# Kernel optimization log

Hardware: AMD Instinct MI355X
Metric: run time of the kernel (lower is better)

The kernel has to match this reference:

```python
import jax, jax.numpy as jnp
import numpy as np

B, T, D = 4, 4096, 4096
G, C, K, M = 1, 4, 128, 32          # num_groups, n_splits, dw_hidden_dim, heads_per_group
I2 = 4                               # qkw inner dim = 2 * dynamic_hidden_dim (dyn_hidden = 32//16 = 2)
EPS = 1.1920929e-07                  # torch F.rms_norm default eps for fp32


def _rms_norm(x):
    # F.rms_norm over last dim, no learned scale
    return x * jax.lax.rsqrt(jnp.mean(x * x, axis=-1, keepdims=True) + EPS)


def setup_inputs() -> dict:
    key = jax.random.key(0)
    k0, k1, k2, k3 = jax.random.split(key, 4)
    dw1_std = np.sqrt(2.0 / (D + K))
    qkw_std = 0.02 / (np.sqrt(2 * 32 * 2) * (32 + 2))
    dd_std = 0.05 * np.sqrt(2.0 / (32 + D))
    return {
        "query_vec": jax.random.normal(k0, (B, T, D), dtype=jnp.float32),
        "dw1": jax.random.normal(k1, (D, G, C, K), dtype=jnp.float32) * dw1_std,
        "qkw": jax.random.normal(k2, (G, C, K, I2, M), dtype=jnp.float32) * qkw_std,
        "dd": jax.random.normal(k3, (D, G, M * C), dtype=jnp.float32) * dd_std,
        "norm_scale": jnp.ones((G,), dtype=jnp.float32) * 0.001,
    }


def reference(query_vec, dw1, qkw, dd, norm_scale):
    # dw_hidden: [B,T,G,C,K]
    dw_hidden = jnp.einsum('btd,dgck->btgck', query_vec, dw1)
    dw_hidden = jax.nn.gelu(dw_hidden, approximate=False)  # torch nn.GELU() is exact
    # w: [B,T,G,C,I2,M]
    w = jnp.einsum('btgck,gckim->btgcim', dw_hidden, qkw)
    half = qkw.shape[-2] // 2
    w1 = _rms_norm(w[..., :half, :])
    w2 = _rms_norm(w[..., half:, :]) * norm_scale  # norm_scale [G]=(1,) broadcasts over M
    # squeeze group dim (keep_group_dim=False) -> [B,T,C,I,M]
    w1 = w1[:, :, 0]
    w2 = w2[:, :, 0]
    # unbind along C: order pre_q, pre_k, post_q, post_k; key-wise pieces are discarded
    pre_qw1, post_qw1 = w1[:, :, 0], w1[:, :, 2]
    pre_qw2, post_qw2 = w2[:, :, 0], w2[:, :, 2]
    # dd: [B,T,G,M*C] -> tanh -> squeeze G -> split 4
    dd_out = jnp.tanh(jnp.einsum('btd,dgm->btgm', query_vec, dd))[:, :, 0]
    pre_qdd = dd_out[..., 0 * M:1 * M]
    post_qdd = dd_out[..., 2 * M:3 * M]
    # pack all live outputs into one array [B, T, 2*(2*I*M) + 2*M]
    flat = lambda a: a.reshape(a.shape[0], a.shape[1], -1)
    return jnp.concatenate(
        [flat(pre_qw1), flat(pre_qw2), pre_qdd,
         flat(post_qw1), flat(post_qw2), post_qdd], axis=-1)
```

## Files before the change

### kernel.cpp

```cpp
#include <hip/hip_runtime.h>
#include <cstdint>
#include <cstddef>

typedef __bf16 bf16x8 __attribute__((ext_vector_type(8)));
typedef float f32x4 __attribute__((ext_vector_type(4)));

#define D_DIM 4096
#define NCOL 320
#define BM 64
#define NKT 128
#define EPS_F 1.1920929e-07f
#define HS 136
#define STG 28672
#define RING 4
#define SMEM (RING * STG)

__device__ __forceinline__ void gld16(const void* g, void* l) {
  __builtin_amdgcn_global_load_lds(
      (const __attribute__((address_space(1))) unsigned int*)g,
      (__attribute__((address_space(3))) unsigned int*)l,
      16, 0, 0);
}

__global__ void dwp_pack(const float* __restrict__ dw1,
                         const float* __restrict__ qkw,
                         const float* __restrict__ dd,
                         __bf16* __restrict__ Wp,
                         __bf16* __restrict__ Qt) {
  const int b = blockIdx.x;
  const int t = threadIdx.x;
  if (b < 128) {
    __shared__ __bf16 tile[10240];
    const int kt = b;
    const int kk = t >> 3;
    const int d = kt * 32 + kk;
    const int u = kk >> 3;
#pragma unroll
    for (int j = 0; j < 5; ++j) {
      const int n0 = ((t & 7) + j * 8) * 8;
      const float* src;
      if (n0 < 128)      src = dw1 + (size_t)d * 512 + n0;
      else if (n0 < 256) src = dw1 + (size_t)d * 512 + 128 + n0;
      else if (n0 < 288) src = dd + (size_t)d * 128 + (n0 - 256);
      else               src = dd + (size_t)d * 128 + (n0 - 224);
      f32x4 v0 = *(const f32x4*)src;
      f32x4 v1 = *(const f32x4*)(src + 4);
#pragma unroll
      for (int q = 0; q < 8; ++q) {
        const int n = n0 + q;
        const int pos = n * 32 + ((u ^ ((n >> 1) & 3)) << 3) + (kk & 7);
        tile[pos] = (__bf16)((q < 4) ? v0[q] : v1[q - 4]);
      }
    }
    __syncthreads();
    __bf16* dst = Wp + (size_t)kt * 10240;
#pragma unroll
    for (int k = 0; k < 5; ++k) {
      const int u16 = t + k * 256;
      *(bf16x8*)(dst + u16 * 8) = *(const bf16x8*)(tile + u16 * 8);
    }
  } else {
#pragma unroll
    for (int ii = 0; ii < 16; ++ii) {
      const int q = t + ii * 256;
      const int c2 = q >> 11;
      const int rem = q & 2047;
      const int n = rem >> 4;
      const int k0 = (rem & 15) * 8;
      const float* src = qkw + (size_t)c2 * 32768 + (size_t)k0 * 128 + n;
      bf16x8 v;
#pragma unroll
      for (int j = 0; j < 8; ++j) v[j] = (__bf16)src[(size_t)j * 128];
      *(bf16x8*)(Qt + (size_t)c2 * 16384 + (size_t)n * 128 + k0) = v;
    }
  }
}

__global__ __launch_bounds__(512, 2) void dwp_main(
    const float* __restrict__ X,
    const __bf16* __restrict__ Wp,
    const __bf16* __restrict__ Qt,
    const float* __restrict__ NS,
    float* __restrict__ Out) {
  extern __shared__ __align__(16) unsigned char lds[];
  const int t = threadIdx.x;
  const int w = t >> 6;
  const int l = t & 63;
  const int lq = l >> 4;
  const int lm = l & 15;
  const int m0 = blockIdx.x * BM;

  const float* gA = X + (size_t)(m0 + (t >> 3)) * D_DIM +
                    (size_t)(((t & 7) ^ ((t >> 3) & 7)) * 4);

  const int rbase = (w & 1) * 32;
  const int cbase = (w >> 1) * 80;

  unsigned aoff0[2], aoff1[2], boff[5];
#pragma unroll
  for (int rt = 0; rt < 2; ++rt) {
    const int row = rbase + rt * 16 + lm;
    aoff0[rt] = (unsigned)(row * 128 + (((lq * 2 + 0) ^ (lm & 7)) * 16));
    aoff1[rt] = (unsigned)(row * 128 + (((lq * 2 + 1) ^ (lm & 7)) * 16));
  }
#pragma unroll
  for (int ct = 0; ct < 5; ++ct) {
    const int n = cbase + ct * 16 + lm;
    boff[ct] = (unsigned)(8192 + n * 64 + ((lq ^ ((n >> 1) & 3)) << 4));
  }

  f32x4 acc[2][5];
#pragma unroll
  for (int rt = 0; rt < 2; ++rt)
#pragma unroll
    for (int ct = 0; ct < 5; ++ct)
      acc[rt][ct] = (f32x4){0.f, 0.f, 0.f, 0.f};

  auto issue = [&](int kt) {
    unsigned char* base = lds + (kt & 3) * STG;
    const __bf16* wsrc = Wp + (size_t)kt * 10240;
    gld16(gA + (size_t)kt * 32, base + w * 1024);
    gld16(wsrc + (size_t)t * 8, base + 8192 + w * 1024);
    gld16(wsrc + (size_t)(4096 + t * 8), base + 16384 + w * 1024);
    if (w < 4)
      gld16(wsrc + (size_t)(8192 + t * 8), base + 24576 + w * 1024);
  };

  auto body = [&](int kt) {
    const unsigned char* cb = lds + (kt & 3) * STG;
    bf16x8 a[2], b[5];
#pragma unroll
    for (int rt = 0; rt < 2; ++rt) {
      f32x4 x0 = *(const f32x4*)(cb + aoff0[rt]);
      f32x4 x1 = *(const f32x4*)(cb + aoff1[rt]);
#pragma unroll
      for (int j = 0; j < 4; ++j) {
        a[rt][j] = (__bf16)x0[j];
        a[rt][4 + j] = (__bf16)x1[j];
      }
    }
#pragma unroll
    for (int ct = 0; ct < 5; ++ct) b[ct] = *(const bf16x8*)(cb + boff[ct]);
#pragma unroll
    for (int rt = 0; rt < 2; ++rt)
#pragma unroll
      for (int ct = 0; ct < 5; ++ct)
        acc[rt][ct] =
            __builtin_amdgcn_mfma_f32_16x16x32_bf16(a[rt], b[ct], acc[rt][ct], 0, 0, 0);
  };

  issue(0);
  issue(1);
  issue(2);

  for (int kt = 0; kt < NKT - 2; ++kt) {
    if (w < 4) asm volatile("s_waitcnt vmcnt(8) lgkmcnt(0)" ::: "memory");
    else       asm volatile("s_waitcnt vmcnt(6) lgkmcnt(0)" ::: "memory");
    asm volatile("s_barrier" ::: "memory");
    if (kt + 3 < NKT) issue(kt + 3);
    body(kt);
  }
  if (w < 4) asm volatile("s_waitcnt vmcnt(4) lgkmcnt(0)" ::: "memory");
  else       asm volatile("s_waitcnt vmcnt(3) lgkmcnt(0)" ::: "memory");
  asm volatile("s_barrier" ::: "memory");
  body(NKT - 2);
  asm volatile("s_waitcnt vmcnt(0) lgkmcnt(0)" ::: "memory");
  asm volatile("s_barrier" ::: "memory");
  body(NKT - 1);

  __syncthreads();

  const float ns = NS[0];

#pragma unroll
  for (int rt = 0; rt < 2; ++rt) {
#pragma unroll
    for (int ct = 0; ct < 5; ++ct) {
      const int ncol = cbase + ct * 16 + lm;
      const int rowb = rbase + rt * 16 + lq * 4;
      f32x4 v = acc[rt][ct];
      if (ncol < 256) {
        const int c2 = ncol >> 7;
        const int kcol = ncol & 127;
#pragma unroll
        for (int j = 0; j < 4; ++j) {
          float x = v[j];
          float g = 0.5f * x * (1.0f + erff(x * 0.70710678118f));
          *(__bf16*)(lds + (size_t)((c2 * 64 + rowb + j) * HS + kcol) * 2) = (__bf16)g;
        }
      } else {
        const int nd = ncol - 256;
        const int off = (nd < 32) ? (128 + nd) : (256 + nd);
#pragma unroll
        for (int j = 0; j < 4; ++j)
          Out[(size_t)(m0 + rowb + j) * NCOL + off] = tanhf(v[j]);
      }
    }
  }
  __syncthreads();

  const int c2b = w >> 2;
  const int nnb = ((w >> 1) & 1) * 64;
  f32x4 acc2[2][4];
#pragma unroll
  for (int rt = 0; rt < 2; ++rt)
#pragma unroll
    for (int ct = 0; ct < 4; ++ct) acc2[rt][ct] = (f32x4){0.f, 0.f, 0.f, 0.f};

#pragma unroll
  for (int ks = 0; ks < 4; ++ks) {
    bf16x8 a2[2], b2[4];
#pragma unroll
    for (int rt = 0; rt < 2; ++rt)
      a2[rt] = *(const bf16x8*)(lds +
               (size_t)((c2b * 64 + rbase + rt * 16 + lm) * HS + ks * 32 + lq * 8) * 2);
#pragma unroll
    for (int ct = 0; ct < 4; ++ct)
      b2[ct] = *(const bf16x8*)(Qt + (size_t)c2b * 16384 +
               (size_t)(nnb + ct * 16 + lm) * 128 + ks * 32 + lq * 8);
#pragma unroll
    for (int rt = 0; rt < 2; ++rt)
#pragma unroll
      for (int ct = 0; ct < 4; ++ct)
        acc2[rt][ct] =
            __builtin_amdgcn_mfma_f32_16x16x32_bf16(a2[rt], b2[ct], acc2[rt][ct], 0, 0, 0);
  }

#pragma unroll
  for (int rt = 0; rt < 2; ++rt) {
#pragma unroll
    for (int p = 0; p < 2; ++p) {
      const int i = ((w >> 1) & 1) * 2 + p;
      const float sce = (i >= 2) ? ns : 1.0f;
      f32x4 va = acc2[rt][2 * p];
      f32x4 vb = acc2[rt][2 * p + 1];
#pragma unroll
      for (int j = 0; j < 4; ++j) {
        float s = va[j] * va[j] + vb[j] * vb[j];
        s += __shfl_xor(s, 1);
        s += __shfl_xor(s, 2);
        s += __shfl_xor(s, 4);
        s += __shfl_xor(s, 8);
        const float sc = rsqrtf(s * (1.0f / 32.0f) + EPS_F) * sce;
        const size_t row = (size_t)(m0 + rbase + rt * 16 + lq * 4 + j);
        const int off = c2b * 160 + i * 32;
        Out[row * NCOL + off + lm] = va[j] * sc;
        Out[row * NCOL + off + 16 + lm] = vb[j] * sc;
      }
    }
  }
}

extern "C" void kernel_launch(void* const* d_in, const int* in_sizes, int n_in,
                              void* d_out, int out_size, void* d_ws, size_t ws_size,
                              hipStream_t stream) {
  const float* qv  = (const float*)d_in[0];
  const float* dw1 = (const float*)d_in[1];
  const float* qkw = (const float*)d_in[2];
  const float* dd  = (const float*)d_in[3];
  const float* ns  = (const float*)d_in[4];
  float* out = (float*)d_out;

  __bf16* Wp = (__bf16*)d_ws;
  __bf16* Qt = Wp + (size_t)4096 * 320;

  hipFuncSetAttribute((const void*)dwp_main,
                      hipFuncAttributeMaxDynamicSharedMemorySize, SMEM);

  dwp_pack<<<129, 256, 0, stream>>>(dw1, qkw, dd, Wp, Qt);
  dwp_main<<<256, 512, SMEM, stream>>>(qv, Wp, Qt, ns, out);
}
```

Before: 426.5 us.

## Halve row tile to 32 with 256-thread blocks and a 3-stage ring

The main GEMM block shrinks from 64 rows and 8 waves to 32 rows and 4 waves, launching 512 blocks instead of 256. Each wave now owns all 32 rows and an 80-column strip, and the LDS ring shrinks from 4 stages to 3 with a prefetch distance of 2. The explicit lgkmcnt wait is dropped from the loop barrier. The aim is more blocks per CU for latency hiding. In exchange, every block still streams the full weight panel, so weight traffic from L2 doubles and the prefetch depth is shallower.

```diff
diff --git a/kernel.cpp b/kernel.cpp
--- a/kernel.cpp
+++ b/kernel.cpp
@@ -7,12 +7,12 @@
 
 #define D_DIM 4096
 #define NCOL 320
-#define BM 64
+#define BM 32
 #define NKT 128
 #define EPS_F 1.1920929e-07f
 #define HS 136
-#define STG 28672
-#define RING 4
+#define STG 24576
+#define RING 3
 #define SMEM (RING * STG)
 
 __device__ __forceinline__ void gld16(const void* g, void* l) {
@@ -76,7 +76,7 @@
   }
 }
 
-__global__ __launch_bounds__(512, 2) void dwp_main(
+__global__ __launch_bounds__(256, 2) void dwp_main(
     const float* __restrict__ X,
     const __bf16* __restrict__ Wp,
     const __bf16* __restrict__ Qt,
@@ -93,20 +93,19 @@
   const float* gA = X + (size_t)(m0 + (t >> 3)) * D_DIM +
                     (size_t)(((t & 7) ^ ((t >> 3) & 7)) * 4);
 
-  const int rbase = (w & 1) * 32;
-  const int cbase = (w >> 1) * 80;
+  const int cbase = w * 80;
 
   unsigned aoff0[2], aoff1[2], boff[5];
 #pragma unroll
   for (int rt = 0; rt < 2; ++rt) {
-    const int row = rbase + rt * 16 + lm;
+    const int row = rt * 16 + lm;
     aoff0[rt] = (unsigned)(row * 128 + (((lq * 2 + 0) ^ (lm & 7)) * 16));
     aoff1[rt] = (unsigned)(row * 128 + (((lq * 2 + 1) ^ (lm & 7)) * 16));
   }
 #pragma unroll
   for (int ct = 0; ct < 5; ++ct) {
     const int n = cbase + ct * 16 + lm;
-    boff[ct] = (unsigned)(8192 + n * 64 + ((lq ^ ((n >> 1) & 3)) << 4));
+    boff[ct] = (unsigned)(4096 + n * 64 + ((lq ^ ((n >> 1) & 3)) << 4));
   }
 
   f32x4 acc[2][5];
@@ -116,18 +115,18 @@
     for (int ct = 0; ct < 5; ++ct)
       acc[rt][ct] = (f32x4){0.f, 0.f, 0.f, 0.f};
 
-  auto issue = [&](int kt) {
-    unsigned char* base = lds + (kt & 3) * STG;
+  auto issue = [&](int kt, int slot) {
+    unsigned char* base = lds + slot * STG;
     const __bf16* wsrc = Wp + (size_t)kt * 10240;
     gld16(gA + (size_t)kt * 32, base + w * 1024);
-    gld16(wsrc + (size_t)t * 8, base + 8192 + w * 1024);
-    gld16(wsrc + (size_t)(4096 + t * 8), base + 16384 + w * 1024);
-    if (w < 4)
-      gld16(wsrc + (size_t)(8192 + t * 8), base + 24576 + w * 1024);
+#pragma unroll
+    for (int k = 0; k < 5; ++k)
+      gld16(wsrc + (size_t)(k * 2048) + t * 8,
+            base + 4096 + k * 4096 + w * 1024);
   };
 
-  auto body = [&](int kt) {
-    const unsigned char* cb = lds + (kt & 3) * STG;
+  auto body = [&](int kt, int slot) {
+    const unsigned char* cb = lds + slot * STG;
     bf16x8 a[2], b[5];
 #pragma unroll
     for (int rt = 0; rt < 2; ++rt) {
@@ -149,24 +148,23 @@
             __builtin_amdgcn_mfma_f32_16x16x32_bf16(a[rt], b[ct], acc[rt][ct], 0, 0, 0);
   };
 
-  issue(0);
-  issue(1);
-  issue(2);
-
-  for (int kt = 0; kt < NKT - 2; ++kt) {
-    if (w < 4) asm volatile("s_waitcnt vmcnt(8) lgkmcnt(0)" ::: "memory");
-    else       asm volatile("s_waitcnt vmcnt(6) lgkmcnt(0)" ::: "memory");
+  issue(0, 0);
+  issue(1, 1);
+
+  int rb = 0;
+  for (int kt = 0; kt < NKT - 1; ++kt) {
+    asm volatile("s_waitcnt vmcnt(6)" ::: "memory");
     asm volatile("s_barrier" ::: "memory");
-    if (kt + 3 < NKT) issue(kt + 3);
-    body(kt);
-  }
-  if (w < 4) asm volatile("s_waitcnt vmcnt(4) lgkmcnt(0)" ::: "memory");
-  else       asm volatile("s_waitcnt vmcnt(3) lgkmcnt(0)" ::: "memory");
+    if (kt + 2 < NKT) {
+      int ri = rb + 2; if (ri >= RING) ri -= RING;
+      issue(kt + 2, ri);
+    }
+    body(kt, rb);
+    ++rb; if (rb == RING) rb = 0;
+  }
+  asm volatile("s_waitcnt vmcnt(0)" ::: "memory");
   asm volatile("s_barrier" ::: "memory");
-  body(NKT - 2);
-  asm volatile("s_waitcnt vmcnt(0) lgkmcnt(0)" ::: "memory");
-  asm volatile("s_barrier" ::: "memory");
-  body(NKT - 1);
+  body(NKT - 1, rb);
 
   __syncthreads();
 
@@ -177,7 +175,7 @@
 #pragma unroll
     for (int ct = 0; ct < 5; ++ct) {
       const int ncol = cbase + ct * 16 + lm;
-      const int rowb = rbase + rt * 16 + lq * 4;
+      const int rowb = rt * 16 + lq * 4;
       f32x4 v = acc[rt][ct];
       if (ncol < 256) {
         const int c2 = ncol >> 7;
@@ -186,7 +184,7 @@
         for (int j = 0; j < 4; ++j) {
           float x = v[j];
           float g = 0.5f * x * (1.0f + erff(x * 0.70710678118f));
-          *(__bf16*)(lds + (size_t)((c2 * 64 + rowb + j) * HS + kcol) * 2) = (__bf16)g;
+          *(__bf16*)(lds + (size_t)((c2 * 32 + rowb + j) * HS + kcol) * 2) = (__bf16)g;
         }
       } else {
         const int nd = ncol - 256;
@@ -199,8 +197,8 @@
   }
   __syncthreads();
 
-  const int c2b = w >> 2;
-  const int nnb = ((w >> 1) & 1) * 64;
+  const int c2b = w >> 1;
+  const int nnb = (w & 1) * 64;
   f32x4 acc2[2][4];
 #pragma unroll
   for (int rt = 0; rt < 2; ++rt)
@@ -213,7 +211,7 @@
 #pragma unroll
     for (int rt = 0; rt < 2; ++rt)
       a2[rt] = *(const bf16x8*)(lds +
-               (size_t)((c2b * 64 + rbase + rt * 16 + lm) * HS + ks * 32 + lq * 8) * 2);
+               (size_t)((c2b * 32 + rt * 16 + lm) * HS + ks * 32 + lq * 8) * 2);
 #pragma unroll
     for (int ct = 0; ct < 4; ++ct)
       b2[ct] = *(const bf16x8*)(Qt + (size_t)c2b * 16384 +
@@ -230,7 +228,7 @@
   for (int rt = 0; rt < 2; ++rt) {
 #pragma unroll
     for (int p = 0; p < 2; ++p) {
-      const int i = ((w >> 1) & 1) * 2 + p;
+      const int i = (w & 1) * 2 + p;
       const float sce = (i >= 2) ? ns : 1.0f;
       f32x4 va = acc2[rt][2 * p];
       f32x4 vb = acc2[rt][2 * p + 1];
@@ -242,7 +240,7 @@
         s += __shfl_xor(s, 4);
         s += __shfl_xor(s, 8);
         const float sc = rsqrtf(s * (1.0f / 32.0f) + EPS_F) * sce;
-        const size_t row = (size_t)(m0 + rbase + rt * 16 + lq * 4 + j);
+        const size_t row = (size_t)(m0 + rt * 16 + lq * 4 + j);
         const int off = c2b * 160 + i * 32;
         Out[row * NCOL + off + lm] = va[j] * sc;
         Out[row * NCOL + off + 16 + lm] = vb[j] * sc;
@@ -268,5 +266,5 @@
                       hipFuncAttributeMaxDynamicSharedMemorySize, SMEM);
 
   dwp_pack<<<129, 256, 0, stream>>>(dw1, qkw, dd, Wp, Qt);
-  dwp_main<<<256, 512, SMEM, stream>>>(qv, Wp, Qt, ns, out);
-}
+  dwp_main<<<512, 256, SMEM, stream>>>(qv, Wp, Qt, ns, out);
+}
```

Measured after the change: 425.5 us. No clear change (-0.2%).
